# Kernel tuning notes

Measured on AMD Instinct MI355X. Metric: run time of the kernel, lower is better.

Reference implementation:

```python
import jax, jax.numpy as jnp
import numpy as np

L = 2        # rnn_layers
H = 512      # hidden size
T_MAX = 20   # text_max_len
V = 10000    # NUM_WORDS
B = 32       # batch
S = 49       # spatial positions (7x7)


def setup_inputs() -> dict:
    key = jax.random.key(0)
    ks = jax.random.split(key, 12)
    w = lambda k, shape: jax.random.normal(k, shape, dtype=jnp.float32) * 0.02
    return {
        "img_channels": jax.random.normal(ks[0], (B, 512, 7, 7), dtype=jnp.float32),
        "pooled": jax.random.normal(ks[1], (B, H), dtype=jnp.float32),
        "embed_table": w(ks[2], (V, H)),
        "Wq": w(ks[3], (H, H)), "bq": jnp.zeros((H,), jnp.float32),
        "Wk": w(ks[4], (S, S)), "bk": jnp.zeros((S,), jnp.float32),
        "Wv": w(ks[5], (S, S)), "bv": jnp.zeros((S,), jnp.float32),
        "Wih": w(ks[6], (L, 4 * H, H)), "Whh": w(ks[7], (L, 4 * H, H)),
        "bih": jnp.zeros((L, 4 * H), jnp.float32), "bhh": jnp.zeros((L, 4 * H), jnp.float32),
        "projW": w(ks[8], (V, H)), "projb": jnp.zeros((V,), jnp.float32),
        "hattW": w(ks[9], (H, 2 * H)), "hattb": jnp.zeros((H,), jnp.float32),
        "sos_idx": 1,
    }


def _lstm_cell(x, h, c, wih, whh, bi, bh):
    # PyTorch gate order: i, f, g, o
    g = x @ wih.T + bi + h @ whh.T + bh
    i, f, gg, o = jnp.split(g, 4, axis=-1)
    c2 = jax.nn.sigmoid(f) * c + jax.nn.sigmoid(i) * jnp.tanh(gg)
    return jax.nn.sigmoid(o) * jnp.tanh(c2), c2


def reference(img_channels, pooled, embed_table, Wq, bq, Wk, bk, Wv, bv,
              Wih, Whh, bih, bhh, projW, projb, hattW, hattb, sos_idx):
    Bsz = img_channels.shape[0]
    chan = img_channels.reshape(Bsz, 512, -1)           # [B,512,49]
    # keys/values are step-invariant: precompute once
    keys = jnp.tanh(chan @ Wk.T + bk)                    # [B,512,49]
    values = jnp.tanh(chan @ Wv.T + bv)                  # [B,512,49]

    emb0 = jnp.broadcast_to(embed_table[sos_idx], (Bsz, H))   # <SOS> embedding
    h0 = jnp.broadcast_to(pooled[None], (L, Bsz, H))
    c0 = h0

    def step(carry, _):
        emb, h, c = carry
        x = emb
        hs, cs = [], []
        for l in range(L):  # small fixed layer count
            hl, cl = _lstm_cell(x, h[l], c[l], Wih[l], Whh[l], bih[l], bhh[l])
            hs.append(hl); cs.append(cl)
            x = hl
        out = x                                          # [B,H] top-layer output
        h = jnp.stack(hs); c = jnp.stack(cs)
        # greedy next-token embedding (no teacher forcing)
        logits = out @ projW.T + projb                   # [B,V]
        emb_next = embed_table[jnp.argmax(logits, axis=-1)]
        # cross-attention gated hidden update (all layers at once)
        q = jnp.tanh(h @ Wq.T + bq)                      # [L,B,H]
        scores = jnp.einsum('lbd,bds->lbs', q, keys) / 7.0
        w = jax.nn.softmax(scores, axis=-1)              # [L,B,49]
        attn = jnp.einsum('lbs,bds->lbd', w, values)     # [L,B,H]
        h = jnp.tanh(jnp.concatenate([attn, h], axis=-1) @ hattW.T + hattb)
        return (emb_next, h, c), out

    _, outs = jax.lax.scan(step, (emb0, h0, c0), None, length=T_MAX - 1)
    pred = jnp.concatenate([emb0[None], outs], axis=0)   # [T,B,H]
    res = jnp.einsum('tbd,vd->bvt', pred, projW) + projb[None, :, None]
    return res                                           # [B,V,T]
```

## Files before the change

### kernel.cpp

```cpp
#include <hip/hip_runtime.h>

namespace {

constexpr int B = 32, H = 512, L = 2, T = 20, V = 10000, S = 49;

__device__ __forceinline__ float sigf(float x) { return 1.0f / (1.0f + expf(-x)); }
__device__ __forceinline__ float dot4(float4 a, float4 b) {
  return a.x*b.x + a.y*b.y + a.z*b.z + a.w*b.w;
}

__global__ __launch_bounds__(256) void setup_kernel(
    const float* __restrict__ chan,
    const float* __restrict__ Wk, const float* __restrict__ bk,
    const float* __restrict__ Wv, const float* __restrict__ bv,
    float* __restrict__ keysT, float* __restrict__ valuesT,
    const float* __restrict__ pooled, const float* __restrict__ embed,
    const int* __restrict__ sos,
    float* __restrict__ emb, float* __restrict__ h, float* __restrict__ c,
    const float* __restrict__ projW, const float* __restrict__ projb,
    float* __restrict__ slog0) {
  __shared__ __align__(16) float smem[8448];
  int blk = blockIdx.x, tid = threadIdx.x;
  if (blk < 256) {
    float* ch = smem;
    float* wk = smem + 64 * 52;
    float* wv = wk + 49 * 52;
    int b = blk >> 3, dt = blk & 7;
    for (int i = tid; i < 49 * 49; i += 256) {
      int s = i / 49, j = i % 49;
      wk[s * 52 + j] = Wk[i]; wv[s * 52 + j] = Wv[i];
    }
    for (int i = tid; i < 64 * 49; i += 256) {
      int d = i / 49, j = i % 49;
      ch[d * 52 + j] = chan[((size_t)b * 512 + dt * 64 + d) * S + j];
    }
    __syncthreads();
    int dl = tid >> 2, sq = tid & 3;
    for (int s = sq; s < S; s += 4) {
      float ak = bk[s], av = bv[s];
      for (int j = 0; j < 49; ++j) {
        float cv = ch[dl * 52 + j];
        ak += cv * wk[s * 52 + j];
        av += cv * wv[s * 52 + j];
      }
      int d = dt * 64 + dl;
      keysT[((size_t)b * S + s) * H + d] = tanhf(ak);
      valuesT[((size_t)b * S + s) * H + d] = tanhf(av);
    }
  } else if (blk < 384) {
    int idx = (blk - 256) * 256 + tid;
    float p = pooled[idx & (B * H - 1)];
    h[idx] = p;
    c[idx] = p;
    if (idx < B * H) emb[idx] = embed[(size_t)sos[0] * H + (idx & (H - 1))];
  } else {
    float* es = smem;
    es[tid] = embed[(size_t)sos[0] * H + tid];
    es[tid + 256] = embed[(size_t)sos[0] * H + tid + 256];
    __syncthreads();
    int ko = tid & 15, vl = tid >> 4;
    int v = (blk - 384) * 16 + vl;
    const float* wrow = projW + (size_t)v * H;
    float4 w[8];
#pragma unroll
    for (int kk = 0; kk < 8; ++kk) w[kk] = *(const float4*)&wrow[kk * 64 + ko * 4];
    float acc = 0.f;
#pragma unroll
    for (int kk = 0; kk < 8; ++kk)
      acc += dot4(*(const float4*)&es[kk * 64 + ko * 4], w[kk]);
    acc += __shfl_xor(acc, 1);
    acc += __shfl_xor(acc, 2);
    acc += __shfl_xor(acc, 4);
    acc += __shfl_xor(acc, 8);
    if (ko == 0) {
      float r = acc + projb[v];
      for (int b = 0; b < 32; ++b) slog0[(size_t)b * V + v] = r;
    }
  }
}

__global__ __launch_bounds__(256) void lstm_kernel(
    const float* __restrict__ x, const float* __restrict__ hprev,
    const float* __restrict__ cprev,
    const float* __restrict__ Wih, const float* __restrict__ Whh,
    const float* __restrict__ bih, const float* __restrict__ bhh,
    float* __restrict__ hout, float* __restrict__ cout) {
  __shared__ __align__(16) float smem[32 * 512];
  int tid = threadIdx.x;
  int hi = blockIdx.x;
  int ko = tid & 15, rr = (tid >> 4) & 3, bh = tid >> 6;
  {
    const float4* xg = (const float4*)x;
    float4* s4 = (float4*)smem;
    for (int i = tid; i < 4096; i += 256) s4[i] = xg[i];
  }
  __syncthreads();
  float acc[8];
#pragma unroll
  for (int j = 0; j < 8; ++j) acc[j] = 0.f;
  {
    const float* wrow = Wih + ((size_t)rr * H + hi) * H;
    float4 w[8];
#pragma unroll
    for (int kk = 0; kk < 8; ++kk) w[kk] = *(const float4*)&wrow[kk * 64 + ko * 4];
#pragma unroll
    for (int j = 0; j < 8; ++j) {
      const float* xb = smem + (bh * 8 + j) * 512;
#pragma unroll
      for (int kk = 0; kk < 8; ++kk)
        acc[j] += dot4(*(const float4*)&xb[kk * 64 + ko * 4], w[kk]);
    }
  }
  __syncthreads();
  {
    const float4* hg = (const float4*)hprev;
    float4* s4 = (float4*)smem;
    for (int i = tid; i < 4096; i += 256) s4[i] = hg[i];
  }
  __syncthreads();
  {
    const float* wrow = Whh + ((size_t)rr * H + hi) * H;
    float4 w[8];
#pragma unroll
    for (int kk = 0; kk < 8; ++kk) w[kk] = *(const float4*)&wrow[kk * 64 + ko * 4];
#pragma unroll
    for (int j = 0; j < 8; ++j) {
      const float* xb = smem + (bh * 8 + j) * 512;
#pragma unroll
      for (int kk = 0; kk < 8; ++kk)
        acc[j] += dot4(*(const float4*)&xb[kk * 64 + ko * 4], w[kk]);
    }
  }
  __syncthreads();
#pragma unroll
  for (int j = 0; j < 8; ++j) {
    acc[j] += __shfl_xor(acc[j], 1);
    acc[j] += __shfl_xor(acc[j], 2);
    acc[j] += __shfl_xor(acc[j], 4);
    acc[j] += __shfl_xor(acc[j], 8);
  }
  float* gbuf = smem;
  if (ko == 0) {
    float bias = bih[rr * H + hi] + bhh[rr * H + hi];
#pragma unroll
    for (int j = 0; j < 8; ++j) gbuf[rr * 32 + bh * 8 + j] = acc[j] + bias;
  }
  __syncthreads();
  if (tid < 32) {
    int b = tid;
    float gi = gbuf[b], gf = gbuf[32 + b], gg = gbuf[64 + b], go = gbuf[96 + b];
    float c2 = sigf(gf) * cprev[b * H + hi] + sigf(gi) * tanhf(gg);
    hout[b * H + hi] = sigf(go) * tanhf(c2);
    cout[b * H + hi] = c2;
  }
}

__global__ __launch_bounds__(256) void projsat_kernel(
    const float* __restrict__ hmid_all,
    const float* __restrict__ projW, const float* __restrict__ projb,
    const float* __restrict__ Wq, const float* __restrict__ bq,
    const float* __restrict__ keysT, const float* __restrict__ valuesT,
    float* __restrict__ dst, float* __restrict__ cat) {
  __shared__ __align__(16) float smem[32 * 512];
  int blk = blockIdx.x, tid = threadIdx.x;
  if (blk < 625) {
    const float* xin = hmid_all + B * H;
    {
      const float4* xg = (const float4*)xin;
      float4* s4 = (float4*)smem;
      for (int i = tid; i < 4096; i += 256) s4[i] = xg[i];
    }
    __syncthreads();
    int ko = tid & 15, vl = tid >> 4;
    int v = blk * 16 + vl;
    const float* wrow = projW + (size_t)v * H;
    float4 w[8];
#pragma unroll
    for (int kk = 0; kk < 8; ++kk) w[kk] = *(const float4*)&wrow[kk * 64 + ko * 4];
    float acc[32];
#pragma unroll
    for (int b = 0; b < 32; ++b) acc[b] = 0.f;
    for (int b = 0; b < 32; ++b) {
      const float* xb = smem + b * 512;
#pragma unroll
      for (int kk = 0; kk < 8; ++kk)
        acc[b] += dot4(*(const float4*)&xb[kk * 64 + ko * 4], w[kk]);
    }
#pragma unroll
    for (int b = 0; b < 32; ++b) {
      acc[b] += __shfl_xor(acc[b], 1);
      acc[b] += __shfl_xor(acc[b], 2);
      acc[b] += __shfl_xor(acc[b], 4);
      acc[b] += __shfl_xor(acc[b], 8);
    }
    if (ko == 0) {
      float bias = projb[v];
      for (int b = 0; b < 32; ++b) dst[(size_t)b * V + v] = acc[b] + bias;
    }
  } else {
    int lb = blk - 625;
    int b = lb & 31, lg = lb >> 5;
    float* hr  = smem;
    float* qv  = smem + 512;
    float* scl = smem + 1040;
    float* wts = smem + 1104;
    const float* hrow = hmid_all + (size_t)lg * B * H + (size_t)b * H;
    hr[tid] = hrow[tid];
    hr[tid + 256] = hrow[tid + 256];
    __syncthreads();
    int ko = tid & 15, vl = tid >> 4;
    for (int jg = 0; jg < 32; ++jg) {
      int j = jg * 16 + vl;
      const float* wrow = Wq + (size_t)j * H;
      float4 w[8];
#pragma unroll
      for (int kk = 0; kk < 8; ++kk) w[kk] = *(const float4*)&wrow[kk * 64 + ko * 4];
      float acc = 0.f;
#pragma unroll
      for (int kk = 0; kk < 8; ++kk)
        acc += dot4(*(const float4*)&hr[kk * 64 + ko * 4], w[kk]);
      acc += __shfl_xor(acc, 1);
      acc += __shfl_xor(acc, 2);
      acc += __shfl_xor(acc, 4);
      acc += __shfl_xor(acc, 8);
      if (ko == 0) qv[(j >> 7) * 132 + (j & 127)] = tanhf(acc + bq[j]);
    }
    __syncthreads();
    int kq = tid & 3, sl = tid >> 2;
    float acc = 0.f;
    if (sl < S) {
      const float* kr = keysT + ((size_t)b * S + sl) * H + kq * 128;
      const float* qr = &qv[kq * 132];
      for (int k = 0; k < 128; k += 4)
        acc += dot4(*(const float4*)&qr[k], *(const float4*)&kr[k]);
    }
    acc += __shfl_xor(acc, 1);
    acc += __shfl_xor(acc, 2);
    if (kq == 0 && sl < S) scl[sl] = acc * (1.0f / 7.0f);
    __syncthreads();
    if (tid < 64) {
      float sc = (tid < S) ? scl[tid] : -3.4e38f;
      float m = sc;
      for (int o = 32; o > 0; o >>= 1) m = fmaxf(m, __shfl_xor(m, o));
      float e = (tid < S) ? expf(sc - m) : 0.f;
      float sum = e;
      for (int o = 32; o > 0; o >>= 1) sum += __shfl_xor(sum, o);
      if (tid < S) wts[tid] = e / sum;
    }
    __syncthreads();
    float acc0 = 0.f, acc1 = 0.f;
    for (int s = 0; s < S; ++s) {
      float w = wts[s];
      const float* vr = valuesT + ((size_t)b * S + s) * H;
      acc0 += w * vr[tid];
      acc1 += w * vr[tid + 256];
    }
    cat[lb * 1024 + tid] = acc0;
    cat[lb * 1024 + tid + 256] = acc1;
    cat[lb * 1024 + 512 + tid] = hmid_all[lb * H + tid];
    cat[lb * 1024 + 768 + tid] = hmid_all[lb * H + tid + 256];
  }
}

__global__ __launch_bounds__(256) void hattarg_kernel(
    const float* __restrict__ cat, const float* __restrict__ hattW,
    const float* __restrict__ hattb, float* __restrict__ h,
    const float* __restrict__ logits, const float* __restrict__ embed,
    float* __restrict__ emb) {
  __shared__ __align__(16) float smem[16 * 1024];
  int blk = blockIdx.x, tid = threadIdx.x;
  if (blk < 128) {
    int lbg = blk & 3, jg = blk >> 2;
    {
      const float4* cg2 = (const float4*)(cat + lbg * 16 * 1024);
      float4* s4 = (float4*)smem;
      for (int i = tid; i < 4096; i += 256) s4[i] = cg2[i];
    }
    __syncthreads();
    int ko = tid & 15, jl = tid >> 4;
    int j = jg * 16 + jl;
    const float* wrow = hattW + (size_t)j * 1024;
    float4 w[16];
#pragma unroll
    for (int kk = 0; kk < 16; ++kk) w[kk] = *(const float4*)&wrow[kk * 64 + ko * 4];
    float acc[16];
#pragma unroll
    for (int lb = 0; lb < 16; ++lb) acc[lb] = 0.f;
    for (int lb = 0; lb < 16; ++lb) {
      const float* cb = smem + lb * 1024;
#pragma unroll
      for (int kk = 0; kk < 16; ++kk)
        acc[lb] += dot4(*(const float4*)&cb[kk * 64 + ko * 4], w[kk]);
    }
#pragma unroll
    for (int lb = 0; lb < 16; ++lb) {
      acc[lb] += __shfl_xor(acc[lb], 1);
      acc[lb] += __shfl_xor(acc[lb], 2);
      acc[lb] += __shfl_xor(acc[lb], 4);
      acc[lb] += __shfl_xor(acc[lb], 8);
    }
    if (ko == 0) {
      float bias = hattb[j];
      for (int lb = 0; lb < 16; ++lb)
        h[(lbg * 16 + lb) * H + j] = tanhf(acc[lb] + bias);
    }
  } else {
    int b = blk - 128;
    float* sv = smem;
    int* si = (int*)(smem + 256);
    float best = -3.4e38f;
    int bi = 0x7fffffff;
    for (int it = 0; it < 10; ++it) {
      int v0 = it * 1024 + tid * 4;
      if (v0 < V) {
        float4 lv = *(const float4*)&logits[(size_t)b * V + v0];
        if (lv.x > best) { best = lv.x; bi = v0; }
        if (lv.y > best) { best = lv.y; bi = v0 + 1; }
        if (lv.z > best) { best = lv.z; bi = v0 + 2; }
        if (lv.w > best) { best = lv.w; bi = v0 + 3; }
      }
    }
    sv[tid] = best; si[tid] = bi;
    __syncthreads();
    for (int st = 128; st > 0; st >>= 1) {
      if (tid < st) {
        float ov = sv[tid + st]; int oi = si[tid + st];
        if (ov > sv[tid] || (ov == sv[tid] && oi < si[tid])) { sv[tid] = ov; si[tid] = oi; }
      }
      __syncthreads();
    }
    int idx = si[0];
    for (int i = tid; i < H; i += 256) emb[b * H + i] = embed[(size_t)idx * H + i];
  }
}

__global__ __launch_bounds__(256) void finalize_kernel(
    const float* __restrict__ slog, float* __restrict__ outp) {
  int idx = blockIdx.x * 256 + threadIdx.x;
  float vals[T];
#pragma unroll
  for (int t = 0; t < T; ++t) vals[t] = slog[(size_t)t * (B * V) + idx];
#pragma unroll
  for (int t = 0; t < T; t += 4)
    *(float4*)&outp[(size_t)idx * T + t] =
        make_float4(vals[t], vals[t + 1], vals[t + 2], vals[t + 3]);
}


__global__ __launch_bounds__(256) void kv_kernel(
    const float* __restrict__ chan,
    const float* __restrict__ Wk, const float* __restrict__ bk,
    const float* __restrict__ Wv, const float* __restrict__ bv,
    float* __restrict__ keysT, float* __restrict__ valuesT) {
  __shared__ float ch[64][52];
  __shared__ float wk[49][52], wv[49][52];
  int b = blockIdx.x >> 3, dt = blockIdx.x & 7;
  int tid = threadIdx.x;
  for (int i = tid; i < 49 * 49; i += 256) {
    int s = i / 49, j = i % 49;
    wk[s][j] = Wk[i]; wv[s][j] = Wv[i];
  }
  for (int i = tid; i < 64 * 49; i += 256) {
    int d = i / 49, j = i % 49;
    ch[d][j] = chan[((size_t)b * 512 + dt * 64 + d) * S + j];
  }
  __syncthreads();
  int dl = tid >> 2, sq = tid & 3;
  for (int s = sq; s < S; s += 4) {
    float ak = bk[s], av = bv[s];
    for (int j = 0; j < 49; ++j) {
      float cv = ch[dl][j];
      ak += cv * wk[s][j];
      av += cv * wv[s][j];
    }
    int d = dt * 64 + dl;
    keysT[((size_t)b * S + s) * H + d] = tanhf(ak);
    valuesT[((size_t)b * S + s) * H + d] = tanhf(av);
  }
}

__global__ void init_kernel(const float* __restrict__ pooled,
                            const float* __restrict__ embed,
                            const int* __restrict__ sos,
                            float* __restrict__ emb, float* __restrict__ h,
                            float* __restrict__ c) {
  int idx = blockIdx.x * 256 + threadIdx.x;
  float p = pooled[idx & (B * H - 1)];
  h[idx] = p;
  c[idx] = p;
  if (idx < B * H) emb[idx] = embed[sos[0] * H + (idx & (H - 1))];
}

__global__ __launch_bounds__(256) void projq_kernel(
    const float* __restrict__ xin,
    const float* __restrict__ projW, const float* __restrict__ projb,
    float* __restrict__ logits, float* __restrict__ ocol, int direct, int tcol,
    const float* __restrict__ hmid_all, const float* __restrict__ Wq,
    const float* __restrict__ bq, float* __restrict__ q) {
  __shared__ __align__(16) float xs[32 * 512];
  int blk = blockIdx.x, tid = threadIdx.x;
  int ko = tid & 15, vl = tid >> 4;
  if (blk < 625) {
    {
      const float4* xg = (const float4*)xin;
      float4* s4 = (float4*)xs;
      for (int i = tid; i < 4096; i += 256) s4[i] = xg[i];
    }
    __syncthreads();
    int v = blk * 16 + vl;
    const float* wrow = projW + (size_t)v * H;
    float4 w[8];
#pragma unroll
    for (int kk = 0; kk < 8; ++kk) w[kk] = *(const float4*)&wrow[kk * 64 + ko * 4];
    float acc[32];
#pragma unroll
    for (int b = 0; b < 32; ++b) acc[b] = 0.f;
    for (int b = 0; b < 32; ++b) {
      const float* xb = xs + b * 512;
#pragma unroll
      for (int kk = 0; kk < 8; ++kk)
        acc[b] += dot4(*(const float4*)&xb[kk * 64 + ko * 4], w[kk]);
    }
#pragma unroll
    for (int b = 0; b < 32; ++b) {
      acc[b] += __shfl_xor(acc[b], 1);
      acc[b] += __shfl_xor(acc[b], 2);
      acc[b] += __shfl_xor(acc[b], 4);
      acc[b] += __shfl_xor(acc[b], 8);
    }
    if (ko == 0) {
      float bias = projb[v];
      for (int b = 0; b < 32; ++b) {
        float r = acc[b] + bias;
        logits[b * V + v] = r;
        if (direct) ocol[((size_t)b * V + v) * T + tcol] = r;
        else        ocol[b * V + v] = r;
      }
    }
  } else {
    int b2 = blk - 625;
    int lg = b2 & 1, jg = b2 >> 1;
    {
      const float4* xg = (const float4*)(hmid_all + lg * 32 * H);
      float4* s4 = (float4*)xs;
      for (int i = tid; i < 4096; i += 256) s4[i] = xg[i];
    }
    __syncthreads();
    int j = jg * 16 + vl;
    const float* wrow = Wq + (size_t)j * H;
    float4 w[8];
#pragma unroll
    for (int kk = 0; kk < 8; ++kk) w[kk] = *(const float4*)&wrow[kk * 64 + ko * 4];
    float acc[32];
#pragma unroll
    for (int b = 0; b < 32; ++b) acc[b] = 0.f;
    for (int b = 0; b < 32; ++b) {
      const float* xb = xs + b * 512;
#pragma unroll
      for (int kk = 0; kk < 8; ++kk)
        acc[b] += dot4(*(const float4*)&xb[kk * 64 + ko * 4], w[kk]);
    }
#pragma unroll
    for (int b = 0; b < 32; ++b) {
      acc[b] += __shfl_xor(acc[b], 1);
      acc[b] += __shfl_xor(acc[b], 2);
      acc[b] += __shfl_xor(acc[b], 4);
      acc[b] += __shfl_xor(acc[b], 8);
    }
    if (ko == 0) {
      float bias = bq[j];
      for (int b = 0; b < 32; ++b)
        q[(lg * 32 + b) * H + j] = tanhf(acc[b] + bias);
    }
  }
}

__global__ __launch_bounds__(256) void sattn_kernel(
    const float* __restrict__ q, const float* __restrict__ keysT,
    const float* __restrict__ valuesT, const float* __restrict__ hmid,
    float* __restrict__ cat) {
  __shared__ __align__(16) float qv[528];
  __shared__ float scl[64];
  __shared__ float wts[64];
  int lb = blockIdx.x, tid = threadIdx.x;
  int b = lb & 31;
  {
    int c0 = tid, c1 = tid + 256;
    qv[(c0 >> 7) * 132 + (c0 & 127)] = q[lb * H + c0];
    qv[(c1 >> 7) * 132 + (c1 & 127)] = q[lb * H + c1];
  }
  __syncthreads();
  int kq = tid & 3, sl = tid >> 2;
  float acc = 0.f;
  if (sl < S) {
    const float* kr = keysT + ((size_t)b * S + sl) * H + kq * 128;
    const float* qr = &qv[kq * 132];
    for (int k = 0; k < 128; k += 4)
      acc += dot4(*(const float4*)&qr[k], *(const float4*)&kr[k]);
  }
  acc += __shfl_xor(acc, 1);
  acc += __shfl_xor(acc, 2);
  if (kq == 0 && sl < S) scl[sl] = acc * (1.0f / 7.0f);
  __syncthreads();
  if (tid < 64) {
    float sc = (tid < S) ? scl[tid] : -3.4e38f;
    float m = sc;
    for (int o = 32; o > 0; o >>= 1) m = fmaxf(m, __shfl_xor(m, o));
    float e = (tid < S) ? expf(sc - m) : 0.f;
    float sum = e;
    for (int o = 32; o > 0; o >>= 1) sum += __shfl_xor(sum, o);
    if (tid < S) wts[tid] = e / sum;
  }
  __syncthreads();
  float acc0 = 0.f, acc1 = 0.f;
  for (int s = 0; s < S; ++s) {
    float w = wts[s];
    const float* vr = valuesT + ((size_t)b * S + s) * H;
    acc0 += w * vr[tid];
    acc1 += w * vr[tid + 256];
  }
  cat[lb * 1024 + tid] = acc0;
  cat[lb * 1024 + tid + 256] = acc1;
  cat[lb * 1024 + 512 + tid] = hmid[lb * H + tid];
  cat[lb * 1024 + 768 + tid] = hmid[lb * H + tid + 256];
}

}

extern "C" void kernel_launch(void* const* d_in, const int* in_sizes, int n_in,
                              void* d_out, int out_size, void* d_ws, size_t ws_size,
                              hipStream_t stream) {
  (void)in_sizes; (void)n_in; (void)out_size;
  const float* chan   = (const float*)d_in[0];
  const float* pooled = (const float*)d_in[1];
  const float* embed  = (const float*)d_in[2];
  const float* Wq     = (const float*)d_in[3];
  const float* bq     = (const float*)d_in[4];
  const float* Wk     = (const float*)d_in[5];
  const float* bk     = (const float*)d_in[6];
  const float* Wv     = (const float*)d_in[7];
  const float* bv     = (const float*)d_in[8];
  const float* Wih    = (const float*)d_in[9];
  const float* Whh    = (const float*)d_in[10];
  const float* bih    = (const float*)d_in[11];
  const float* bhh    = (const float*)d_in[12];
  const float* projW  = (const float*)d_in[13];
  const float* projb  = (const float*)d_in[14];
  const float* hattW  = (const float*)d_in[15];
  const float* hattb  = (const float*)d_in[16];
  const int*   sos    = (const int*)d_in[17];

  float* out = (float*)d_out;
  float* ws  = (float*)d_ws;

  float* keysT   = ws;
  float* valuesT = keysT + B * S * 512;
  float* emb     = valuesT + B * S * 512;
  float* h       = emb + B * H;
  float* c       = h + L * B * H;
  float* hmid    = c + L * B * H;
  float* cat     = hmid + L * B * H;
  float* q       = cat + L * B * 1024;
  float* logits  = q + L * B * H;
  float* slog    = logits + B * V;

  size_t base_floats = (size_t)(slog - ws);
  bool staged = ws_size >= (base_floats + (size_t)T * B * V) * sizeof(float);

  if (staged) {
    setup_kernel<<<1009, 256, 0, stream>>>(chan, Wk, bk, Wv, bv, keysT, valuesT,
                                           pooled, embed, sos, emb, h, c,
                                           projW, projb, slog);
    for (int t = 0; t < T - 1; ++t) {
      float* dst = slog + (size_t)(t + 1) * B * V;
      lstm_kernel<<<512, 256, 0, stream>>>(emb, h, c, Wih, Whh, bih, bhh, hmid, c);
      lstm_kernel<<<512, 256, 0, stream>>>(hmid, h + B * H, c + B * H,
                                           Wih + 4 * H * H, Whh + 4 * H * H,
                                           bih + 4 * H, bhh + 4 * H,
                                           hmid + B * H, c + B * H);
      bool last = (t == T - 2);
      projsat_kernel<<<last ? 625 : 689, 256, 0, stream>>>(
          hmid, projW, projb, Wq, bq, keysT, valuesT, dst, cat);
      if (!last)
        hattarg_kernel<<<160, 256, 0, stream>>>(cat, hattW, hattb, h,
                                                dst, embed, emb);
    }
    finalize_kernel<<<(B * V) / 256, 256, 0, stream>>>(slog, out);
    return;
  }

  kv_kernel<<<256, 256, 0, stream>>>(chan, Wk, bk, Wv, bv, keysT, valuesT);
  init_kernel<<<(L * B * H) / 256, 256, 0, stream>>>(pooled, embed, sos, emb, h, c);
  projq_kernel<<<625, 256, 0, stream>>>(emb, projW, projb, logits, out,
                                        1, 0, hmid, Wq, bq, q);
  for (int t = 0; t < T - 1; ++t) {
    lstm_kernel<<<512, 256, 0, stream>>>(emb, h, c, Wih, Whh, bih, bhh, hmid, c);
    lstm_kernel<<<512, 256, 0, stream>>>(hmid, h + B * H, c + B * H,
                                         Wih + 4 * H * H, Whh + 4 * H * H,
                                         bih + 4 * H, bhh + 4 * H,
                                         hmid + B * H, c + B * H);
    projq_kernel<<<689, 256, 0, stream>>>(hmid + B * H, projW, projb, logits, out,
                                          1, t + 1, hmid, Wq, bq, q);
    sattn_kernel<<<L * B, 256, 0, stream>>>(q, keysT, valuesT, hmid, cat);
    hattarg_kernel<<<160, 256, 0, stream>>>(cat, hattW, hattb, h,
                                            logits, embed, emb);
  }
}
```

Measured before the change: 2.035 ms.

## Split batch across blocks and read activations directly from global instead of LDS

The LSTM, projection and hidden-attention GEMV kernels now split the batch dimension in half across twice as many blocks. They also drop the large shared-memory staging of activations and read activation rows straight from global memory, which the L2 cache should serve. This aims to raise occupancy and parallelism, since the old 64KB LDS footprint limited resident blocks, and to remove staging barriers. The cost is that each weight row is loaded by two blocks, and activation reads repeat per block instead of being shared from LDS. The old kernels are kept as fallbacks for the non-staged path.

Result: slower. 2.229 ms (+9.5%).

```diff
diff --git a/kernel.cpp b/kernel.cpp
--- a/kernel.cpp
+++ b/kernel.cpp
@@ -85,70 +85,56 @@
     const float* __restrict__ Wih, const float* __restrict__ Whh,
     const float* __restrict__ bih, const float* __restrict__ bhh,
     float* __restrict__ hout, float* __restrict__ cout) {
-  __shared__ __align__(16) float smem[32 * 512];
+  __shared__ float gbuf[64];
   int tid = threadIdx.x;
-  int hi = blockIdx.x;
+  int hi = blockIdx.x >> 1, half = blockIdx.x & 1;
   int ko = tid & 15, rr = (tid >> 4) & 3, bh = tid >> 6;
-  {
-    const float4* xg = (const float4*)x;
-    float4* s4 = (float4*)smem;
-    for (int i = tid; i < 4096; i += 256) s4[i] = xg[i];
-  }
-  __syncthreads();
-  float acc[8];
-#pragma unroll
-  for (int j = 0; j < 8; ++j) acc[j] = 0.f;
+  float acc[4];
+#pragma unroll
+  for (int j = 0; j < 4; ++j) acc[j] = 0.f;
+  float4 w[8];
   {
     const float* wrow = Wih + ((size_t)rr * H + hi) * H;
-    float4 w[8];
 #pragma unroll
     for (int kk = 0; kk < 8; ++kk) w[kk] = *(const float4*)&wrow[kk * 64 + ko * 4];
-#pragma unroll
-    for (int j = 0; j < 8; ++j) {
-      const float* xb = smem + (bh * 8 + j) * 512;
-#pragma unroll
-      for (int kk = 0; kk < 8; ++kk)
-        acc[j] += dot4(*(const float4*)&xb[kk * 64 + ko * 4], w[kk]);
-    }
-  }
-  __syncthreads();
-  {
-    const float4* hg = (const float4*)hprev;
-    float4* s4 = (float4*)smem;
-    for (int i = tid; i < 4096; i += 256) s4[i] = hg[i];
-  }
-  __syncthreads();
+  }
+#pragma unroll
+  for (int j = 0; j < 4; ++j) {
+    int b = half * 16 + bh * 4 + j;
+    const float* xb = x + (size_t)b * H;
+#pragma unroll
+    for (int kk = 0; kk < 8; ++kk)
+      acc[j] += dot4(*(const float4*)&xb[kk * 64 + ko * 4], w[kk]);
+  }
   {
     const float* wrow = Whh + ((size_t)rr * H + hi) * H;
-    float4 w[8];
 #pragma unroll
     for (int kk = 0; kk < 8; ++kk) w[kk] = *(const float4*)&wrow[kk * 64 + ko * 4];
-#pragma unroll
-    for (int j = 0; j < 8; ++j) {
-      const float* xb = smem + (bh * 8 + j) * 512;
-#pragma unroll
-      for (int kk = 0; kk < 8; ++kk)
-        acc[j] += dot4(*(const float4*)&xb[kk * 64 + ko * 4], w[kk]);
-    }
-  }
-  __syncthreads();
-#pragma unroll
-  for (int j = 0; j < 8; ++j) {
+  }
+#pragma unroll
+  for (int j = 0; j < 4; ++j) {
+    int b = half * 16 + bh * 4 + j;
+    const float* hb = hprev + (size_t)b * H;
+#pragma unroll
+    for (int kk = 0; kk < 8; ++kk)
+      acc[j] += dot4(*(const float4*)&hb[kk * 64 + ko * 4], w[kk]);
+  }
+#pragma unroll
+  for (int j = 0; j < 4; ++j) {
     acc[j] += __shfl_xor(acc[j], 1);
     acc[j] += __shfl_xor(acc[j], 2);
     acc[j] += __shfl_xor(acc[j], 4);
     acc[j] += __shfl_xor(acc[j], 8);
   }
-  float* gbuf = smem;
   if (ko == 0) {
     float bias = bih[rr * H + hi] + bhh[rr * H + hi];
 #pragma unroll
-    for (int j = 0; j < 8; ++j) gbuf[rr * 32 + bh * 8 + j] = acc[j] + bias;
-  }
-  __syncthreads();
-  if (tid < 32) {
-    int b = tid;
-    float gi = gbuf[b], gf = gbuf[32 + b], gg = gbuf[64 + b], go = gbuf[96 + b];
+    for (int j = 0; j < 4; ++j) gbuf[rr * 16 + bh * 4 + j] = acc[j] + bias;
+  }
+  __syncthreads();
+  if (tid < 16) {
+    int b = half * 16 + tid;
+    float gi = gbuf[tid], gf = gbuf[16 + tid], gg = gbuf[32 + tid], go = gbuf[48 + tid];
     float c2 = sigf(gf) * cprev[b * H + hi] + sigf(gi) * tanhf(gg);
     hout[b * H + hi] = sigf(go) * tanhf(c2);
     cout[b * H + hi] = c2;
@@ -161,44 +147,41 @@
     const float* __restrict__ Wq, const float* __restrict__ bq,
     const float* __restrict__ keysT, const float* __restrict__ valuesT,
     float* __restrict__ dst, float* __restrict__ cat) {
-  __shared__ __align__(16) float smem[32 * 512];
+  __shared__ __align__(16) float smem[1168];
   int blk = blockIdx.x, tid = threadIdx.x;
-  if (blk < 625) {
+  if (blk < 1250) {
     const float* xin = hmid_all + B * H;
-    {
-      const float4* xg = (const float4*)xin;
-      float4* s4 = (float4*)smem;
-      for (int i = tid; i < 4096; i += 256) s4[i] = xg[i];
-    }
-    __syncthreads();
+    int vchunk = blk >> 1, half = blk & 1;
     int ko = tid & 15, vl = tid >> 4;
-    int v = blk * 16 + vl;
+    int v = vchunk * 16 + vl;
     const float* wrow = projW + (size_t)v * H;
     float4 w[8];
 #pragma unroll
     for (int kk = 0; kk < 8; ++kk) w[kk] = *(const float4*)&wrow[kk * 64 + ko * 4];
-    float acc[32];
-#pragma unroll
-    for (int b = 0; b < 32; ++b) acc[b] = 0.f;
-    for (int b = 0; b < 32; ++b) {
-      const float* xb = smem + b * 512;
+    float acc[16];
+#pragma unroll
+    for (int bl = 0; bl < 16; ++bl) acc[bl] = 0.f;
+#pragma unroll 4
+    for (int bl = 0; bl < 16; ++bl) {
+      const float* xb = xin + (size_t)(half * 16 + bl) * H;
 #pragma unroll
       for (int kk = 0; kk < 8; ++kk)
-        acc[b] += dot4(*(const float4*)&xb[kk * 64 + ko * 4], w[kk]);
-    }
-#pragma unroll
-    for (int b = 0; b < 32; ++b) {
-      acc[b] += __shfl_xor(acc[b], 1);
-      acc[b] += __shfl_xor(acc[b], 2);
-      acc[b] += __shfl_xor(acc[b], 4);
-      acc[b] += __shfl_xor(acc[b], 8);
+        acc[bl] += dot4(*(const float4*)&xb[kk * 64 + ko * 4], w[kk]);
+    }
+#pragma unroll
+    for (int bl = 0; bl < 16; ++bl) {
+      acc[bl] += __shfl_xor(acc[bl], 1);
+      acc[bl] += __shfl_xor(acc[bl], 2);
+      acc[bl] += __shfl_xor(acc[bl], 4);
+      acc[bl] += __shfl_xor(acc[bl], 8);
     }
     if (ko == 0) {
       float bias = projb[v];
-      for (int b = 0; b < 32; ++b) dst[(size_t)b * V + v] = acc[b] + bias;
+      for (int bl = 0; bl < 16; ++bl)
+        dst[(size_t)(half * 16 + bl) * V + v] = acc[bl] + bias;
     }
   } else {
-    int lb = blk - 625;
+    int lb = blk - 1250;
     int b = lb & 31, lg = lb >> 5;
     float* hr  = smem;
     float* qv  = smem + 512;
@@ -267,45 +250,40 @@
     const float* __restrict__ hattb, float* __restrict__ h,
     const float* __restrict__ logits, const float* __restrict__ embed,
     float* __restrict__ emb) {
-  __shared__ __align__(16) float smem[16 * 1024];
+  __shared__ __align__(16) float smem[512];
   int blk = blockIdx.x, tid = threadIdx.x;
-  if (blk < 128) {
-    int lbg = blk & 3, jg = blk >> 2;
-    {
-      const float4* cg2 = (const float4*)(cat + lbg * 16 * 1024);
-      float4* s4 = (float4*)smem;
-      for (int i = tid; i < 4096; i += 256) s4[i] = cg2[i];
-    }
-    __syncthreads();
+  if (blk < 256) {
+    int lbg = blk & 7, jg = blk >> 3;
     int ko = tid & 15, jl = tid >> 4;
     int j = jg * 16 + jl;
     const float* wrow = hattW + (size_t)j * 1024;
     float4 w[16];
 #pragma unroll
     for (int kk = 0; kk < 16; ++kk) w[kk] = *(const float4*)&wrow[kk * 64 + ko * 4];
-    float acc[16];
-#pragma unroll
-    for (int lb = 0; lb < 16; ++lb) acc[lb] = 0.f;
-    for (int lb = 0; lb < 16; ++lb) {
-      const float* cb = smem + lb * 1024;
+    float acc[8];
+#pragma unroll
+    for (int ll = 0; ll < 8; ++ll) acc[ll] = 0.f;
+#pragma unroll 2
+    for (int ll = 0; ll < 8; ++ll) {
+      const float* cb = cat + (size_t)(lbg * 8 + ll) * 1024;
 #pragma unroll
       for (int kk = 0; kk < 16; ++kk)
-        acc[lb] += dot4(*(const float4*)&cb[kk * 64 + ko * 4], w[kk]);
-    }
-#pragma unroll
-    for (int lb = 0; lb < 16; ++lb) {
-      acc[lb] += __shfl_xor(acc[lb], 1);
-      acc[lb] += __shfl_xor(acc[lb], 2);
-      acc[lb] += __shfl_xor(acc[lb], 4);
-      acc[lb] += __shfl_xor(acc[lb], 8);
+        acc[ll] += dot4(*(const float4*)&cb[kk * 64 + ko * 4], w[kk]);
+    }
+#pragma unroll
+    for (int ll = 0; ll < 8; ++ll) {
+      acc[ll] += __shfl_xor(acc[ll], 1);
+      acc[ll] += __shfl_xor(acc[ll], 2);
+      acc[ll] += __shfl_xor(acc[ll], 4);
+      acc[ll] += __shfl_xor(acc[ll], 8);
     }
     if (ko == 0) {
       float bias = hattb[j];
-      for (int lb = 0; lb < 16; ++lb)
-        h[(lbg * 16 + lb) * H + j] = tanhf(acc[lb] + bias);
+      for (int ll = 0; ll < 8; ++ll)
+        h[(size_t)(lbg * 8 + ll) * H + j] = tanhf(acc[ll] + bias);
     }
   } else {
-    int b = blk - 128;
+    int b = blk - 256;
     float* sv = smem;
     int* si = (int*)(smem + 256);
     float best = -3.4e38f;
@@ -389,6 +367,82 @@
   h[idx] = p;
   c[idx] = p;
   if (idx < B * H) emb[idx] = embed[sos[0] * H + (idx & (H - 1))];
+}
+
+__global__ __launch_bounds__(256) void lstm_kernel_fb(
+    const float* __restrict__ x, const float* __restrict__ hprev,
+    const float* __restrict__ cprev,
+    const float* __restrict__ Wih, const float* __restrict__ Whh,
+    const float* __restrict__ bih, const float* __restrict__ bhh,
+    float* __restrict__ hout, float* __restrict__ cout) {
+  __shared__ __align__(16) float smem[32 * 512];
+  int tid = threadIdx.x;
+  int hi = blockIdx.x;
+  int ko = tid & 15, rr = (tid >> 4) & 3, bh = tid >> 6;
+  {
+    const float4* xg = (const float4*)x;
+    float4* s4 = (float4*)smem;
+    for (int i = tid; i < 4096; i += 256) s4[i] = xg[i];
+  }
+  __syncthreads();
+  float acc[8];
+#pragma unroll
+  for (int j = 0; j < 8; ++j) acc[j] = 0.f;
+  {
+    const float* wrow = Wih + ((size_t)rr * H + hi) * H;
+    float4 w[8];
+#pragma unroll
+    for (int kk = 0; kk < 8; ++kk) w[kk] = *(const float4*)&wrow[kk * 64 + ko * 4];
+#pragma unroll
+    for (int j = 0; j < 8; ++j) {
+      const float* xb = smem + (bh * 8 + j) * 512;
+#pragma unroll
+      for (int kk = 0; kk < 8; ++kk)
+        acc[j] += dot4(*(const float4*)&xb[kk * 64 + ko * 4], w[kk]);
+    }
+  }
+  __syncthreads();
+  {
+    const float4* hg = (const float4*)hprev;
+    float4* s4 = (float4*)smem;
+    for (int i = tid; i < 4096; i += 256) s4[i] = hg[i];
+  }
+  __syncthreads();
+  {
+    const float* wrow = Whh + ((size_t)rr * H + hi) * H;
+    float4 w[8];
+#pragma unroll
+    for (int kk = 0; kk < 8; ++kk) w[kk] = *(const float4*)&wrow[kk * 64 + ko * 4];
+#pragma unroll
+    for (int j = 0; j < 8; ++j) {
+      const float* xb = smem + (bh * 8 + j) * 512;
+#pragma unroll
+      for (int kk = 0; kk < 8; ++kk)
+        acc[j] += dot4(*(const float4*)&xb[kk * 64 + ko * 4], w[kk]);
+    }
+  }
+  __syncthreads();
+#pragma unroll
+  for (int j = 0; j < 8; ++j) {
+    acc[j] += __shfl_xor(acc[j], 1);
+    acc[j] += __shfl_xor(acc[j], 2);
+    acc[j] += __shfl_xor(acc[j], 4);
+    acc[j] += __shfl_xor(acc[j], 8);
+  }
+  float* gbuf = smem;
+  if (ko == 0) {
+    float bias = bih[rr * H + hi] + bhh[rr * H + hi];
+#pragma unroll
+    for (int j = 0; j < 8; ++j) gbuf[rr * 32 + bh * 8 + j] = acc[j] + bias;
+  }
+  __syncthreads();
+  if (tid < 32) {
+    int b = tid;
+    float gi = gbuf[b], gf = gbuf[32 + b], gg = gbuf[64 + b], go = gbuf[96 + b];
+    float c2 = sigf(gf) * cprev[b * H + hi] + sigf(gi) * tanhf(gg);
+    hout[b * H + hi] = sigf(go) * tanhf(c2);
+    cout[b * H + hi] = c2;
+  }
 }
 
 __global__ __launch_bounds__(256) void projq_kernel(
@@ -523,6 +577,78 @@
   cat[lb * 1024 + tid + 256] = acc1;
   cat[lb * 1024 + 512 + tid] = hmid[lb * H + tid];
   cat[lb * 1024 + 768 + tid] = hmid[lb * H + tid + 256];
+}
+
+__global__ __launch_bounds__(256) void hattarg_kernel_fb(
+    const float* __restrict__ cat, const float* __restrict__ hattW,
+    const float* __restrict__ hattb, float* __restrict__ h,
+    const float* __restrict__ logits, const float* __restrict__ embed,
+    float* __restrict__ emb) {
+  __shared__ __align__(16) float smem[16 * 1024];
+  int blk = blockIdx.x, tid = threadIdx.x;
+  if (blk < 128) {
+    int lbg = blk & 3, jg = blk >> 2;
+    {
+      const float4* cg2 = (const float4*)(cat + lbg * 16 * 1024);
+      float4* s4 = (float4*)smem;
+      for (int i = tid; i < 4096; i += 256) s4[i] = cg2[i];
+    }
+    __syncthreads();
+    int ko = tid & 15, jl = tid >> 4;
+    int j = jg * 16 + jl;
+    const float* wrow = hattW + (size_t)j * 1024;
+    float4 w[16];
+#pragma unroll
+    for (int kk = 0; kk < 16; ++kk) w[kk] = *(const float4*)&wrow[kk * 64 + ko * 4];
+    float acc[16];
+#pragma unroll
+    for (int lb = 0; lb < 16; ++lb) acc[lb] = 0.f;
+    for (int lb = 0; lb < 16; ++lb) {
+      const float* cb = smem + lb * 1024;
+#pragma unroll
+      for (int kk = 0; kk < 16; ++kk)
+        acc[lb] += dot4(*(const float4*)&cb[kk * 64 + ko * 4], w[kk]);
+    }
+#pragma unroll
+    for (int lb = 0; lb < 16; ++lb) {
+      acc[lb] += __shfl_xor(acc[lb], 1);
+      acc[lb] += __shfl_xor(acc[lb], 2);
+      acc[lb] += __shfl_xor(acc[lb], 4);
+      acc[lb] += __shfl_xor(acc[lb], 8);
+    }
+    if (ko == 0) {
+      float bias = hattb[j];
+      for (int lb = 0; lb < 16; ++lb)
+        h[(lbg * 16 + lb) * H + j] = tanhf(acc[lb] + bias);
+    }
+  } else {
+    int b = blk - 128;
+    float* sv = smem;
+    int* si = (int*)(smem + 256);
+    float best = -3.4e38f;
+    int bi = 0x7fffffff;
+    for (int it = 0; it < 10; ++it) {
+      int v0 = it * 1024 + tid * 4;
+      if (v0 < V) {
+        float4 lv = *(const float4*)&logits[b * V + v0];
+        if (lv.x > best) { best = lv.x; bi = v0; }
+        if (lv.y > best) { best = lv.y; bi = v0 + 1; }
+        if (lv.z > best) { best = lv.z; bi = v0 + 2; }
+        if (lv.w > best) { best = lv.w; bi = v0 + 3; }
+      }
+    }
+    sv[tid] = best; si[tid] = bi;
+    __syncthreads();
+    for (int st = 128; st > 0; st >>= 1) {
+      if (tid < st) {
+        float ov = sv[tid + st]; int oi = si[tid + st];
+        if (ov > sv[tid] || (ov == sv[tid] && oi < si[tid])) { sv[tid] = ov; si[tid] = oi; }
+      }
+      __syncthreads();
+    }
+    int idx = si[0];
+    for (int i = tid; i < H; i += 256) emb[b * H + i] = embed[(size_t)idx * H + i];
+  }
 }
 
 }
@@ -573,16 +699,16 @@
                                            projW, projb, slog);
     for (int t = 0; t < T - 1; ++t) {
       float* dst = slog + (size_t)(t + 1) * B * V;
-      lstm_kernel<<<512, 256, 0, stream>>>(emb, h, c, Wih, Whh, bih, bhh, hmid, c);
-      lstm_kernel<<<512, 256, 0, stream>>>(hmid, h + B * H, c + B * H,
-                                           Wih + 4 * H * H, Whh + 4 * H * H,
-                                           bih + 4 * H, bhh + 4 * H,
-                                           hmid + B * H, c + B * H);
+      lstm_kernel<<<1024, 256, 0, stream>>>(emb, h, c, Wih, Whh, bih, bhh, hmid, c);
+      lstm_kernel<<<1024, 256, 0, stream>>>(hmid, h + B * H, c + B * H,
+                                            Wih + 4 * H * H, Whh + 4 * H * H,
+                                            bih + 4 * H, bhh + 4 * H,
+                                            hmid + B * H, c + B * H);
       bool last = (t == T - 2);
-      projsat_kernel<<<last ? 625 : 689, 256, 0, stream>>>(
+      projsat_kernel<<<last ? 1250 : 1314, 256, 0, stream>>>(
           hmid, projW, projb, Wq, bq, keysT, valuesT, dst, cat);
       if (!last)
-        hattarg_kernel<<<160, 256, 0, stream>>>(cat, hattW, hattb, h,
+        hattarg_kernel<<<288, 256, 0, stream>>>(cat, hattW, hattb, h,
                                                 dst, embed, emb);
     }
     finalize_kernel<<<(B * V) / 256, 256, 0, stream>>>(slog, out);
@@ -594,15 +720,15 @@
   projq_kernel<<<625, 256, 0, stream>>>(emb, projW, projb, logits, out,
                                         1, 0, hmid, Wq, bq, q);
   for (int t = 0; t < T - 1; ++t) {
-    lstm_kernel<<<512, 256, 0, stream>>>(emb, h, c, Wih, Whh, bih, bhh, hmid, c);
-    lstm_kernel<<<512, 256, 0, stream>>>(hmid, h + B * H, c + B * H,
-                                         Wih + 4 * H * H, Whh + 4 * H * H,
-                                         bih + 4 * H, bhh + 4 * H,
-                                         hmid + B * H, c + B * H);
+    lstm_kernel_fb<<<512, 256, 0, stream>>>(emb, h, c, Wih, Whh, bih, bhh, hmid, c);
+    lstm_kernel_fb<<<512, 256, 0, stream>>>(hmid, h + B * H, c + B * H,
+                                            Wih + 4 * H * H, Whh + 4 * H * H,
+                                            bih + 4 * H, bhh + 4 * H,
+                                            hmid + B * H, c + B * H);
     projq_kernel<<<689, 256, 0, stream>>>(hmid + B * H, projW, projb, logits, out,
                                           1, t + 1, hmid, Wq, bq, q);
     sattn_kernel<<<L * B, 256, 0, stream>>>(q, keysT, valuesT, hmid, cat);
-    hattarg_kernel<<<160, 256, 0, stream>>>(cat, hattW, hattb, h,
-                                            logits, embed, emb);
-  }
-}
+    hattarg_kernel_fb<<<160, 256, 0, stream>>>(cat, hattW, hattb, h,
+                                               logits, embed, emb);
+  }
+}
```
